# Kernel optimization log

Hardware: AMD Instinct MI355X
Metric: run time of the kernel (lower is better)

## Reference

```python
import jax, jax.numpy as jnp
import numpy as np

B, T, S, D, H, F, L = 4, 512, 512, 1024, 16, 4096, 2
VOCAB, MAXC = 32000, 1024
PAD, CONCEPT, DBPEDIA, USER = 0, 1, 2, 3
EPS = 1e-5
NEG = -1e20


def _ln(x):
    # LayerNorm (gamma=1, beta=0 at init, as in nn.LayerNorm defaults)
    m = jnp.mean(x, axis=-1, keepdims=True)
    v = jnp.mean((x - m) ** 2, axis=-1, keepdims=True)
    return (x - m) / jnp.sqrt(v + EPS)


def _mha(q_in, kv, mask, Wq, bq, Wk, bk, Wv, bv, Wo, bo):
    # q_in: [B,T,D]; kv: [B,K,D]; mask: broadcastable to [B,H,T,K] (bool)
    dh = D // H

    def heads(x, W, b):
        y = x @ W + b
        return y.reshape(x.shape[0], x.shape[1], H, dh).transpose(0, 2, 1, 3)

    q = heads(q_in, Wq, bq) / jnp.sqrt(jnp.asarray(dh, q_in.dtype))
    k = heads(kv, Wk, bk)
    v = heads(kv, Wv, bv)
    scores = jnp.einsum('bhqd,bhkd->bhqk', q, k)
    # original: dot_prod *= mask; masked_fill(mask==0, -NEAR_INF) == where(mask, s, NEG)
    scores = jnp.where(mask, scores, NEG)
    w = jax.nn.softmax(scores, axis=-1)
    out = jnp.einsum('bhqk,bhkd->bhqd', w, v)
    out = out.transpose(0, 2, 1, 3).reshape(q_in.shape[0], q_in.shape[1], D)
    return out @ Wo + bo


def setup_inputs() -> dict:
    key = jax.random.key(0)
    ks = jax.random.split(key, 16)
    w = 0.02
    return {
        'sum_embeddings': jax.random.normal(ks[0], (VOCAB, D), jnp.float32),
        'predict_vector': jax.random.randint(ks[1], (B, T), 0, VOCAB),
        'encoder_latent_emb': jax.random.normal(ks[2], (B, S, D), jnp.float32),
        'con_graph_fc_emb': jax.random.normal(ks[3], (B, S, D), jnp.float32),
        'db_graph_fc_emb': jax.random.normal(ks[4], (B, S, D), jnp.float32),
        'user_graph_fc_emb': jax.random.normal(ks[5], (B, S, D), jnp.float32),
        'context_mask': jax.random.randint(ks[6], (B, S), 0, 5),
        'pos_emb': jax.random.normal(ks[7], (MAXC, D), jnp.float32) * (D ** -0.5),
        'attn_Wq': jax.random.normal(ks[8], (L, 5, D, D), jnp.float32) * w,
        'attn_bq': jnp.zeros((L, 5, D), jnp.float32),
        'attn_Wk': jax.random.normal(ks[9], (L, 5, D, D), jnp.float32) * w,
        'attn_bk': jnp.zeros((L, 5, D), jnp.float32),
        'attn_Wv': jax.random.normal(ks[10], (L, 5, D, D), jnp.float32) * w,
        'attn_bv': jnp.zeros((L, 5, D), jnp.float32),
        'attn_Wo': jax.random.normal(ks[11], (L, 5, D, D), jnp.float32) * w,
        'attn_bo': jnp.zeros((L, 5, D), jnp.float32),
        'ffn_W1': jax.random.normal(ks[12], (L, D, F), jnp.float32) * w,
        'ffn_b1': jnp.zeros((L, F), jnp.float32),
        'ffn_W2': jax.random.normal(ks[13], (L, F, D), jnp.float32) * w,
        'ffn_b2': jnp.zeros((L, D), jnp.float32),
    }


def reference(sum_embeddings, predict_vector, encoder_latent_emb, con_graph_fc_emb,
              db_graph_fc_emb, user_graph_fc_emb, context_mask, pos_emb,
              attn_Wq, attn_bq, attn_Wk, attn_bk, attn_Wv, attn_bv, attn_Wo, attn_bo,
              ffn_W1, ffn_b1, ffn_W2, ffn_b2):
    enc_mask = (context_mask != PAD)[:, None, None, :]      # [B,1,1,S]
    con_mask = (context_mask != CONCEPT)[:, None, None, :]
    db_mask = (context_mask != DBPEDIA)[:, None, None, :]
    user_mask = (context_mask != USER)[:, None, None, :]
    dec_mask = jnp.tril(jnp.ones((T, T), bool))[None, None]  # causal [1,1,T,T]

    x = sum_embeddings[predict_vector] * jnp.sqrt(jnp.asarray(D, jnp.float32))
    x = x + pos_emb[:T][None]
    x = _ln(x)  # dropout is identity at inference

    for l in range(L):
        def att(i, q, kv, m):
            return _mha(q, kv, m,
                        attn_Wq[l, i], attn_bq[l, i], attn_Wk[l, i], attn_bk[l, i],
                        attn_Wv[l, i], attn_bv[l, i], attn_Wo[l, i], attn_bo[l, i])
        x = _ln(x + att(0, x, x, dec_mask))                      # self
        x = _ln(x + att(1, x, db_graph_fc_emb, db_mask))         # db
        x = _ln(x + att(2, x, con_graph_fc_emb, con_mask))       # kg/concept
        x = _ln(x + att(3, x, user_graph_fc_emb, user_mask))     # user
        x = _ln(x + att(4, x, encoder_latent_emb, enc_mask))     # encoder
        h = jax.nn.relu(x @ ffn_W1[l] + ffn_b1[l]) @ ffn_W2[l] + ffn_b2[l]
        x = _ln(x + h)
    return x
```

## Files before the change

kernel.cpp:

```cpp
#include <hip/hip_runtime.h>

#define BB  4
#define TT  512
#define DD  1024
#define HH  16
#define DHH 64
#define FF  4096

typedef unsigned short u16;
typedef __attribute__((ext_vector_type(8))) short bfrag8;
typedef __attribute__((ext_vector_type(4))) float facc4;

__device__ __forceinline__ u16 f2bf(float f){
  unsigned u = __float_as_uint(f);
  unsigned r = u + 0x7fffu + ((u >> 16) & 1u);
  return (u16)(r >> 16);
}
__device__ __forceinline__ float bf2f(u16 h){
  return __uint_as_float(((unsigned)h) << 16);
}

__device__ __forceinline__ void gload16(const u16* g, u16* l){
  __builtin_amdgcn_global_load_lds(
      (const __attribute__((address_space(1))) void*)g,
      (__attribute__((address_space(3))) void*)l, 16, 0, 0);
}

template<int N> __device__ __forceinline__ void vwait(){
  static_assert(N==0 || N==4 || N==6 || N==8 || N==12, "bad vmcnt literal");
  if constexpr (N==0)  asm volatile("s_waitcnt vmcnt(0)" ::: "memory");
  else if constexpr (N==4)  asm volatile("s_waitcnt vmcnt(4)" ::: "memory");
  else if constexpr (N==6)  asm volatile("s_waitcnt vmcnt(6)" ::: "memory");
  else if constexpr (N==8)  asm volatile("s_waitcnt vmcnt(8)" ::: "memory");
  else if constexpr (N==12) asm volatile("s_waitcnt vmcnt(12)" ::: "memory");
}

__global__ __launch_bounds__(256) void prep_all(
    const float* __restrict__ Wq, const float* __restrict__ Wk,
    const float* __restrict__ Wv, const float* __restrict__ Wo,
    const float* __restrict__ W1, const float* __restrict__ W2,
    const float* __restrict__ g_db, const float* __restrict__ g_con,
    const float* __restrict__ g_usr, const float* __restrict__ g_enc,
    u16* __restrict__ dst0,
    u16* __restrict__ kvb0, u16* __restrict__ kvb1,
    u16* __restrict__ kvb2, u16* __restrict__ kvb3,
    const float* __restrict__ emb, const int* __restrict__ pvec,
    const float* __restrict__ pos, u16* __restrict__ xbout)
{
  const int fid = blockIdx.x;
  const int bid = (fid < 14336) ? ((fid & 7) * 1792 + (fid >> 3)) : fid;
  const int tid = threadIdx.x;
  if (bid >= 22528){
    const int row = bid - 22528;
    const int lane = tid & 63, wid = tid >> 6;
    const int idx = pvec[row];
    const int t = row & (TT - 1);
    float4 e = ((const float4*)(emb + (long)idx * DD))[tid];
    float4 p = ((const float4*)(pos + (long)t * DD))[tid];
    float4 x;
    x.x = e.x * 32.0f + p.x; x.y = e.y * 32.0f + p.y;
    x.z = e.z * 32.0f + p.z; x.w = e.w * 32.0f + p.w;
    float s = x.x + x.y + x.z + x.w;
    #pragma unroll
    for (int o = 32; o; o >>= 1) s += __shfl_xor(s, o);
    __shared__ float red[4];
    if (lane == 0) red[wid] = s;
    __syncthreads();
    const float mean = (red[0] + red[1] + red[2] + red[3]) * (1.0f / DD);
    __syncthreads();
    const float dx = x.x - mean, dy = x.y - mean, dz = x.z - mean, dw = x.w - mean;
    float q = dx*dx + dy*dy + dz*dz + dw*dw;
    #pragma unroll
    for (int o = 32; o; o >>= 1) q += __shfl_xor(q, o);
    if (lane == 0) red[wid] = q;
    __syncthreads();
    const float var = (red[0] + red[1] + red[2] + red[3]) * (1.0f / DD);
    const float rstd = rsqrtf(var + 1e-5f);
    ushort4 o4;
    o4.x = f2bf(dx*rstd); o4.y = f2bf(dy*rstd);
    o4.z = f2bf(dz*rstd); o4.w = f2bf(dw*rstd);
    ((ushort4*)(xbout + (long)row * DD))[tid] = o4;
    return;
  }
  if (bid >= 14336){
    const int r = bid - 14336;
    const float* s; u16* d;
    switch (r >> 11){
      case 0: s = g_db;  d = kvb0; break;
      case 1: s = g_con; d = kvb1; break;
      case 2: s = g_usr; d = kvb2; break;
      default: s = g_enc; d = kvb3; break;
    }
    const int i = (r & 2047) * 256 + tid;
    float4 v = ((const float4*)s)[i];
    ushort4 o;
    o.x = f2bf(v.x); o.y = f2bf(v.y); o.z = f2bf(v.z); o.w = f2bf(v.w);
    ((ushort4*)d)[i] = o;
    return;
  }
  constexpr long D2 = (long)DD * DD, DF = (long)DD * FF;
  constexpr long O_Wproj = 0, O_WkvC = 14*D2, O_WoT = 30*D2,
                 O_W1T = 40*D2, O_W2T = 40*D2 + 2*DF;
  const float* src; long soff, doff; int R, C, rem;
  if (bid < 1536){
    const int j = bid / 512;
    src = (j==0) ? Wq : (j==1) ? Wk : Wv;
    const int l = (bid % 512) / 256; rem = bid & 255;
    soff = (long)l * 5 * D2;
    doff = O_Wproj + (long)l * 7 * D2 +
           ((j==0) ? 0L : (j==1) ? 5L*D2 : 6L*D2);
    R = DD; C = DD;
  } else if (bid < 5632){
    const int idx = (bid - 1536) >> 8; rem = bid & 255;
    const int l = idx >> 3, ci = (idx >> 1) & 3, kv = idx & 1;
    src = kv ? Wv : Wk;
    soff = (long)(l*5 + 1 + ci) * D2;
    doff = O_WkvC + (long)(l*8 + ci*2 + kv) * D2;
    R = DD; C = DD;
  } else if (bid < 7680){
    const int idx = (bid - 5632) >> 8; rem = bid & 255;
    const int l = idx >> 2, ci = idx & 3;
    src = Wq;
    soff = (long)(l*5 + 1 + ci) * D2;
    doff = O_Wproj + (long)l * 7 * D2 + (long)(1 + ci) * D2;
    R = DD; C = DD;
  } else if (bid < 10240){
    const int idx = (bid - 7680) >> 8; rem = bid & 255;
    src = Wo; soff = (long)idx * D2; doff = O_WoT + (long)idx * D2;
    R = DD; C = DD;
  } else if (bid < 12288){
    const int b5 = bid - 10240;
    const int z = b5 >> 10; rem = b5 & 1023;
    src = W1; soff = (long)z * DF; doff = O_W1T + (long)z * DF;
    R = DD; C = FF;
  } else {
    const int b6 = bid - 12288;
    const int z = b6 >> 10; rem = b6 & 1023;
    src = W2; soff = (long)z * DF; doff = O_W2T + (long)z * DF;
    R = FF; C = DD;
  }
  const int ctiles = C >> 6;
  const int c0 = (rem % ctiles) << 6;
  const int r0 = (rem / ctiles) << 6;

  __shared__ u16 tile[64][66];
  const int tr = tid >> 4, tc = tid & 15;
  #pragma unroll
  for (int i = 0; i < 4; ++i){
    const int row = tr + i*16;
    float4 v = ((const float4*)(src + soff + (long)(r0 + row)*C + c0))[tc];
    unsigned* t32 = (unsigned*)&tile[row][tc*4];
    t32[0] = (unsigned)f2bf(v.x) | ((unsigned)f2bf(v.y) << 16);
    t32[1] = (unsigned)f2bf(v.z) | ((unsigned)f2bf(v.w) << 16);
  }
  __syncthreads();
  const int ch = tid & 7;
  const int cb = tid >> 3;
  #pragma unroll
  for (int it = 0; it < 2; ++it){
    const int cc = cb + it*32;
    union { int4 v; u16 u[8]; } P;
    #pragma unroll
    for (int j = 0; j < 8; ++j) P.u[j] = tile[ch*8 + j][cc];
    *(int4*)&dst0[doff + (long)(c0 + cc)*R + r0 + ch*8] = P.v;
  }
}

__global__ __launch_bounds__(256) void ln_chain5(
    const float* __restrict__ o5, u16* __restrict__ xb)
{
  const int row = blockIdx.x;
  const int i = threadIdx.x;
  const int lane = i & 63, wid = i >> 6;
  __shared__ float red[4];
  constexpr long NB = (long)2048 * 1024;
  ushort4 x4 = ((const ushort4*)(xb + (long)row * DD))[i];
  float4 x;
  x.x = bf2f(x4.x); x.y = bf2f(x4.y); x.z = bf2f(x4.z); x.w = bf2f(x4.w);
  #pragma unroll
  for (int it = 0; it < 5; ++it){
    float4 o = ((const float4*)(o5 + (long)it * NB + (long)row * DD))[i];
    x.x += o.x; x.y += o.y; x.z += o.z; x.w += o.w;
    float s = x.x + x.y + x.z + x.w;
    #pragma unroll
    for (int off = 32; off; off >>= 1) s += __shfl_xor(s, off);
    if (lane == 0) red[wid] = s;
    __syncthreads();
    const float mean = (red[0] + red[1] + red[2] + red[3]) * (1.0f / DD);
    __syncthreads();
    x.x -= mean; x.y -= mean; x.z -= mean; x.w -= mean;
    float q = x.x*x.x + x.y*x.y + x.z*x.z + x.w*x.w;
    #pragma unroll
    for (int off = 32; off; off >>= 1) q += __shfl_xor(q, off);
    if (lane == 0) red[wid] = q;
    __syncthreads();
    const float var = (red[0] + red[1] + red[2] + red[3]) * (1.0f / DD);
    const float rstd = rsqrtf(var + 1e-5f);
    x.x *= rstd; x.y *= rstd; x.z *= rstd; x.w *= rstd;
    __syncthreads();
  }
  ushort4 o4;
  o4.x = f2bf(x.x); o4.y = f2bf(x.y); o4.z = f2bf(x.z); o4.w = f2bf(x.w);
  ((ushort4*)(xb + (long)row * DD))[i] = o4;
}

__global__ __launch_bounds__(256) void ln_kernel(
    const float* __restrict__ a,
    float* __restrict__ yf, u16* __restrict__ yb)
{
  const int row = blockIdx.x;
  const int i = threadIdx.x;
  const int lane = i & 63, wid = i >> 6;
  float4 x = ((const float4*)(a + (long)row * DD))[i];
  float s = x.x + x.y + x.z + x.w;
  #pragma unroll
  for (int o = 32; o; o >>= 1) s += __shfl_xor(s, o);
  __shared__ float red[4];
  if (lane == 0) red[wid] = s;
  __syncthreads();
  const float mean = (red[0] + red[1] + red[2] + red[3]) * (1.0f / DD);
  __syncthreads();
  const float dx = x.x - mean, dy = x.y - mean, dz = x.z - mean, dw = x.w - mean;
  float q = dx*dx + dy*dy + dz*dz + dw*dw;
  #pragma unroll
  for (int o = 32; o; o >>= 1) q += __shfl_xor(q, o);
  if (lane == 0) red[wid] = q;
  __syncthreads();
  const float var = (red[0] + red[1] + red[2] + red[3]) * (1.0f / DD);
  const float rstd = rsqrtf(var + 1e-5f);
  float4 y; y.x = dx*rstd; y.y = dy*rstd; y.z = dz*rstd; y.w = dw*rstd;
  if (yf) ((float4*)(yf + (long)row * DD))[i] = y;
  if (yb){
    ushort4 o4; o4.x = f2bf(y.x); o4.y = f2bf(y.y); o4.z = f2bf(y.z); o4.w = f2bf(y.w);
    ((ushort4*)(yb + (long)row * DD))[i] = o4;
  }
}

template<bool CAUSAL>
__device__ __forceinline__ void flash_body(
    const u16* Q, const u16* Kt, const u16* Vt,
    const float* biasS, u16* O,
    int qt, int bh, u16 (*Ks)[64*64], u16 (*Vs)[64*64], u16* Ps)
{
  const int b = bh >> 4, h = bh & 15;
  const int tid = threadIdx.x, lane = tid & 63, wid = tid >> 6;
  const int fr = lane & 15, kg = lane >> 4;
  const int srow = tid >> 3;
  const int gcol = ((tid & 7) ^ (srow & 7)) * 8;
  u16* Pw = Ps + wid * 1024;
  const facc4 z4 = {0.0f, 0.0f, 0.0f, 0.0f};

  const long base = (long)bh * (512 * 64);
  const u16* qrow = Q + base + (long)(qt*64 + wid*16 + fr) * 64;
  const bfrag8 aq0 = *(const bfrag8*)(qrow + kg*8);
  const bfrag8 aq1 = *(const bfrag8*)(qrow + 32 + kg*8);

  auto stageKV = [&](int buf, int kt){
    u16* Kd = Ks[buf] + wid * 512;
    u16* Vd = Vs[buf] + wid * 512;
    #pragma unroll
    for (int p = 0; p < 2; ++p)
      gload16(Kt + base + (long)(kt*64 + p*32 + srow) * 64 + gcol, Kd + p*2048);
    #pragma unroll
    for (int p = 0; p < 2; ++p)
      gload16(Vt + base + (long)(p*32 + srow) * 512 + kt*64 + gcol, Vd + p*2048);
  };

  float mrow[4], lrow[4];
  #pragma unroll
  for (int r = 0; r < 4; ++r){ mrow[r] = -3e38f; lrow[r] = 0.0f; }
  facc4 accO[4] = {};

  const int NT = CAUSAL ? (qt + 1) : 8;
  stageKV(0, 0);
  if (NT > 1){ stageKV(1, 1); vwait<4>(); }
  else vwait<0>();
  __builtin_amdgcn_s_barrier();

  for (int kt = 0; kt < NT; ++kt){
    const int cur = kt & 1;
    bfrag8 bk[4][2], bv[4][2];
    #pragma unroll
    for (int j = 0; j < 4; ++j)
      #pragma unroll
      for (int c2 = 0; c2 < 2; ++c2){
        const int po = (((c2*4 + kg) ^ (fr & 7)) * 8);
        bk[j][c2] = *(const bfrag8*)&Ks[cur][(j*16 + fr)*64 + po];
        bv[j][c2] = *(const bfrag8*)&Vs[cur][(j*16 + fr)*64 + po];
      }
    __builtin_amdgcn_sched_barrier(0);
    __builtin_amdgcn_s_barrier();
    if (kt + 2 < NT){ stageKV(cur, kt + 2); vwait<4>(); }
    else vwait<0>();
    __builtin_amdgcn_s_barrier();

    facc4 sc[4];
    __builtin_amdgcn_s_setprio(1);
    #pragma unroll
    for (int j = 0; j < 4; ++j){
      sc[j] = __builtin_amdgcn_mfma_f32_16x16x32_bf16(aq0, bk[j][0], z4, 0, 0, 0);
      sc[j] = __builtin_amdgcn_mfma_f32_16x16x32_bf16(aq1, bk[j][1], sc[j], 0, 0, 0);
    }
    __builtin_amdgcn_s_setprio(0);
    if (CAUSAL){
      const int rowb = qt*64 + wid*16 + kg*4;
      #pragma unroll
      for (int j = 0; j < 4; ++j){
        const int col = kt*64 + j*16 + fr;
        #pragma unroll
        for (int r = 0; r < 4; ++r)
          if (col > rowb + r) sc[j][r] = -1e20f;
      }
    } else {
      #pragma unroll
      for (int j = 0; j < 4; ++j){
        const float bval = biasS[kt*64 + j*16 + fr];
        #pragma unroll
        for (int r = 0; r < 4; ++r) sc[j][r] += bval;
      }
    }
    float tmax[4];
    #pragma unroll
    for (int r = 0; r < 4; ++r)
      tmax[r] = fmaxf(fmaxf(sc[0][r], sc[1][r]), fmaxf(sc[2][r], sc[3][r]));
    #pragma unroll
    for (int o = 1; o < 16; o <<= 1)
      #pragma unroll
      for (int r = 0; r < 4; ++r)
        tmax[r] = fmaxf(tmax[r], __shfl_xor(tmax[r], o));
    bool grow = false;
    #pragma unroll
    for (int r = 0; r < 4; ++r) grow = grow || (tmax[r] > mrow[r] + 8.0f);
    if (__any(grow)){
      float fac[4];
      #pragma unroll
      for (int r = 0; r < 4; ++r){
        const float mn = fmaxf(mrow[r], tmax[r]);
        fac[r] = __expf(mrow[r] - mn);
        mrow[r] = mn;
        lrow[r] *= fac[r];
      }
      #pragma unroll
      for (int f = 0; f < 4; ++f)
        #pragma unroll
        for (int r = 0; r < 4; ++r) accO[f][r] *= fac[r];
    }
    float tsum[4] = {0.0f, 0.0f, 0.0f, 0.0f};
    #pragma unroll
    for (int j = 0; j < 4; ++j)
      #pragma unroll
      for (int r = 0; r < 4; ++r){
        const float p = __expf(sc[j][r] - mrow[r]);
        sc[j][r] = p; tsum[r] += p;
      }
    #pragma unroll
    for (int o = 1; o < 16; o <<= 1)
      #pragma unroll
      for (int r = 0; r < 4; ++r) tsum[r] += __shfl_xor(tsum[r], o);
    #pragma unroll
    for (int r = 0; r < 4; ++r) lrow[r] += tsum[r];

    #pragma unroll
    for (int j = 0; j < 4; ++j)
      #pragma unroll
      for (int r = 0; r < 4; ++r){
        const int row = kg*4 + r;
        const int col = j*16 + fr;
        Pw[row*64 + (((col >> 3) ^ (row & 7)) * 8) + (col & 7)] = f2bf(sc[j][r]);
      }
    bfrag8 ap[2];
    #pragma unroll
    for (int c2 = 0; c2 < 2; ++c2)
      ap[c2] = *(const bfrag8*)&Pw[fr*64 + (((c2*4 + kg) ^ (fr & 7)) * 8)];
    __builtin_amdgcn_s_setprio(1);
    #pragma unroll
    for (int f = 0; f < 4; ++f){
      accO[f] = __builtin_amdgcn_mfma_f32_16x16x32_bf16(ap[0], bv[f][0], accO[f], 0, 0, 0);
      accO[f] = __builtin_amdgcn_mfma_f32_16x16x32_bf16(ap[1], bv[f][1], accO[f], 0, 0, 0);
    }
    __builtin_amdgcn_s_setprio(0);
  }

  #pragma unroll
  for (int f = 0; f < 4; ++f)
    #pragma unroll
    for (int r = 0; r < 4; ++r){
      const int row = kg*4 + r;
      const int col = f*16 + fr;
      Pw[(row*64 + col) ^ ((row & 7) << 3)] = f2bf(accO[f][r] / lrow[r]);
    }
  const int prow = lane >> 2, pch = lane & 3;
  const long orow = (long)(b*512 + qt*64 + wid*16 + prow) * 1024 + h*64;
  #pragma unroll
  for (int it2 = 0; it2 < 2; ++it2){
    const int ch2 = pch + it2*4;
    int4 w4 = *(const int4*)&Pw[(prow*64 + ch2*8) ^ ((prow & 7) << 3)];
    *(int4*)&O[orow + ch2*8] = w4;
  }
}

__global__ __launch_bounds__(256, 3) void flash_all5(
    const u16* __restrict__ Qb5, const u16* __restrict__ Kb,
    const u16* __restrict__ Vtb, const u16* __restrict__ KVcl,
    const int* __restrict__ cmask, u16* __restrict__ O5)
{
  __shared__ __align__(16) u16 Ks[2][64*64];
  __shared__ __align__(16) u16 Vs[2][64*64];
  __shared__ __align__(16) u16 Ps[4*16*64];
  __shared__ float biasS[512];
  const int z = blockIdx.z;
  const int fid = blockIdx.y * 8 + blockIdx.x;
  const int lid = (fid & 7) * 64 + (fid >> 3);
  const int qt = lid & 7, bh = lid >> 3;
  constexpr long NB = (long)2048 * 1024;
  if (z == 0){
    flash_body<true>(Qb5, Kb, Vtb, nullptr, O5, qt, bh, Ks, Vs, Ps);
  } else {
    const int ci = z - 1;
    const int mode = (0x0312 >> (ci*4)) & 0xF;
    const int b = bh >> 4;
    const int tid = threadIdx.x;
    #pragma unroll
    for (int r = 0; r < 2; ++r){
      const int c = r * 256 + tid;
      biasS[c] = (cmask[b * 512 + c] != mode) ? 0.0f : -1e20f;
    }
    __syncthreads();
    flash_body<false>(Qb5 + (long)z * NB,
                      KVcl + (long)(ci*2) * NB, KVcl + (long)(ci*2 + 1) * NB,
                      biasS, O5 + (long)z * NB, qt, bh, Ks, Vs, Ps);
  }
}

#define MODE_F32   0
#define MODE_BF16  1
#define MODE_KV    4
#define MODE_PROJ  6
#define MODE_F32B  7

__device__ __forceinline__ long qk_off(int gm, int gn){
  return (((long)(gm >> 9) * HH + (gn >> 6)) * TT + (gm & (TT-1))) * DHH + (gn & (DHH-1));
}

template<int BM, int BN, int MODE>
__global__ __launch_bounds__(256, 2) void gemm_k(
    const u16* __restrict__ A, const u16* __restrict__ B,
    const float* __restrict__ bias0, const float* __restrict__ bias1,
    const float* __restrict__ bias2,
    float* __restrict__ Cf, u16* __restrict__ Cb0, u16* __restrict__ Cb1,
    u16* __restrict__ Cb2, const u16* __restrict__ resb,
    int K, int lda, int ldb, int ldc,
    int relu, float alpha)
{
  constexpr int BK = 64;
  constexpr int NBUF = (BM == 64 && BN == 64) ? 3 : 2;
  constexpr int ASZ = BM * BK, BSZ = BN * BK;
  __shared__ __align__(16) u16 As[NBUF * ASZ];
  __shared__ __align__(16) u16 Bs[NBUF * BSZ];

  const int gx = gridDim.x, gy = gridDim.y;
  const int nwg = gx * gy * gridDim.z;
  const int fid = (blockIdx.z * gy + blockIdx.y) * gx + blockIdx.x;
  const int cpx = nwg >> 3;
  const int lid = (fid & 7) * cpx + (fid >> 3);
  const int bx = lid % gx;
  const int rem = lid / gx;
  const int by = rem % gy;
  const int z  = rem / gy;

  const u16* Ab;
  const u16* Bb;
  long cbase;
  constexpr long NBA = (long)2048 * 1024;
  constexpr long D2C = (long)DD * DD;
  if constexpr (MODE == MODE_KV){
    const int ci = z >> 2, ll = (z >> 1) & 1, isv = z & 1;
    Ab = A + (long)ci * NBA;
    Bb = B + (long)(ll*8 + ci*2 + isv) * D2C;
    cbase = (long)(ll*8 + ci*2 + isv) * NBA;
  } else if constexpr (MODE == MODE_F32B){
    Ab = A + (long)z * NBA;
    Bb = B + (long)z * D2C;
    cbase = (long)z * NBA;
  } else {
    Ab = A; Bb = B; cbase = 0;
  }
  const int tid = threadIdx.x, lane = tid & 63, wid = tid >> 6;
  const int m0 = by * BM, n0 = bx * BN;
  constexpr int TMW = BM / 2, TNW = BN / 2;
  constexpr int FM = TMW / 16, FN = TNW / 16;
  const int wm = (wid >> 1) * TMW, wn = (wid & 1) * TNW;
  const int fr = lane & 15, kg = lane >> 4;
  facc4 acc[FM][FN] = {};

  const int srow = tid >> 3;
  const int gcol = (((tid & 7) ^ (srow & 7)) * 8);
  constexpr int AP = BM / 32, BP = BN / 32;
  constexpr int LPS = AP + BP;

  auto stage = [&](int buf, int k0){
    u16* Ad = As + buf * ASZ + wid * 512;
    u16* Bd = Bs + buf * BSZ + wid * 512;
    #pragma unroll
    for (int p = 0; p < AP; ++p)
      gload16(Ab + (long)(m0 + p*32 + srow) * lda + (k0 + gcol), Ad + p*2048);
    #pragma unroll
    for (int p = 0; p < BP; ++p)
      gload16(Bb + (long)(n0 + p*32 + srow) * ldb + (k0 + gcol), Bd + p*2048);
  };

  const int nsteps = K / BK;
  stage(0, 0);
  if constexpr (NBUF == 3){
    if (nsteps > 1) stage(1, BK);
    if (nsteps > 2) stage(2, 2*BK);
    if (nsteps > 2) vwait<2*LPS>();
    else if (nsteps > 1) vwait<LPS>();
    else vwait<0>();
  } else {
    if (nsteps > 1){ stage(1, BK); vwait<LPS>(); }
    else vwait<0>();
  }
  __builtin_amdgcn_s_barrier();

  int cur = 0;
  for (int s = 0; s < nsteps; ++s){
    const u16* Ar = As + cur * ASZ;
    const u16* Br = Bs + cur * BSZ;
    bfrag8 af[FM][2], bfv[FN][2];
    #pragma unroll
    for (int i = 0; i < FM; ++i)
      #pragma unroll
      for (int c2 = 0; c2 < 2; ++c2)
        af[i][c2] = *(const bfrag8*)&Ar[(wm + i*16 + fr) * 64 + (((c2*4 + kg) ^ (fr & 7)) * 8)];
    #pragma unroll
    for (int j = 0; j < FN; ++j)
      #pragma unroll
      for (int c2 = 0; c2 < 2; ++c2)
        bfv[j][c2] = *(const bfrag8*)&Br[(wn + j*16 + fr) * 64 + (((c2*4 + kg) ^ (fr & 7)) * 8)];
    __builtin_amdgcn_sched_barrier(0);
    __builtin_amdgcn_s_barrier();
    if constexpr (NBUF == 3){
      if (s + 3 < nsteps){ stage(cur, (s + 3) * BK); vwait<2*LPS>(); }
      else if (s + 2 < nsteps) vwait<LPS>();
      else if (s + 1 < nsteps) vwait<0>();
    } else {
      if (s + 2 < nsteps){ stage(cur, (s + 2) * BK); vwait<LPS>(); }
      else if (s + 1 < nsteps) vwait<0>();
    }
    __builtin_amdgcn_s_barrier();
    #pragma unroll
    for (int i = 0; i < FM; ++i)
      #pragma unroll
      for (int j = 0; j < FN; ++j){
        acc[i][j] = __builtin_amdgcn_mfma_f32_16x16x32_bf16(af[i][0], bfv[j][0], acc[i][j], 0, 0, 0);
        acc[i][j] = __builtin_amdgcn_mfma_f32_16x16x32_bf16(af[i][1], bfv[j][1], acc[i][j], 0, 0, 0);
      }
    cur = (cur == NBUF - 1) ? 0 : cur + 1;
  }

  if constexpr (MODE == MODE_KV || MODE == MODE_PROJ){
    const float* vb = nullptr; u16* vdst = nullptr; int n0e = 0; bool vpath = false;
    if constexpr (MODE == MODE_KV){
      const int ci = z >> 2, ll = (z >> 1) & 1, isv = z & 1;
      if (isv){ vpath = true; vb = bias1 + (long)(ll*5 + ci + 1) * DD; vdst = Cb0 + cbase; n0e = n0; }
    } else {
      if ((n0 >> 10) == 6){ vpath = true; vb = bias2; vdst = Cb2; n0e = n0 - 6144; }
    }
    if (vpath){
      u16* S = Bs;
      #pragma unroll
      for (int j = 0; j < FN; ++j){
        const int nl = wn + j*16 + fr;
        const float bvv = vb[n0e + nl];
        #pragma unroll
        for (int i = 0; i < FM; ++i)
          #pragma unroll
          for (int rr = 0; rr < 4; ++rr){
            const int ml = wm + i*16 + kg*4 + rr;
            S[(nl*BM + ml) ^ ((nl & 7) << 3)] = f2bf(acc[i][j][rr] + bvv);
          }
      }
      __syncthreads();
      constexpr int TPR = 256 / BN;
      constexpr int CPT = BM / (8 * TPR);
      const int n = tid / TPR;
      const int mh = (tid % TPR) * (BM / TPR);
      const long rowoff = (((long)(m0 >> 9) * HH + ((n0e + n) >> 6)) * DHH
                           + ((n0e + n) & 63)) * TT + (m0 & 511) + mh;
      #pragma unroll
      for (int c = 0; c < CPT; ++c){
        int4 w4 = *(const int4*)&S[(n*BM + mh + c*8) ^ ((n & 7) << 3)];
        *(int4*)&vdst[rowoff + c*8] = w4;
      }
      return;
    }
  }

  if constexpr (MODE == MODE_BF16 || MODE == MODE_PROJ || MODE == MODE_KV){
    u16* S = As;
    const float* bp = bias0;
    float sc2 = alpha;
    u16* dst = Cb0;
    int nb = 0;
    constexpr long NBA2 = (long)2048 * 1024;
    if constexpr (MODE == MODE_KV){
      const int ci = z >> 2, ll = (z >> 1) & 1;
      bp = bias0 + (long)(ll*5 + ci + 1) * DD;
    } else if constexpr (MODE == MODE_PROJ){
      const int sect = n0 >> 10;
      nb = n0 & 1023;
      if (sect <= 4){ bp = bias0 + (long)sect * DD; sc2 = 0.125f; dst = Cb0 + (long)sect * NBA2; }
      else          { bp = bias1; sc2 = 1.0f; dst = Cb1; }
    }
    #pragma unroll
    for (int i = 0; i < FM; ++i)
      #pragma unroll
      for (int j = 0; j < FN; ++j){
        const int nl = wn + j*16 + fr;
        float bvv;
        if constexpr (MODE == MODE_PROJ) bvv = bp[nb + nl];
        else bvv = bp ? bp[n0 + nl] : 0.0f;
        #pragma unroll
        for (int rr = 0; rr < 4; ++rr){
          const int ml = wm + i*16 + kg*4 + rr;
          float v = (acc[i][j][rr] + bvv) * sc2;
          if (relu) v = fmaxf(v, 0.0f);
          S[(ml*BN + nl) ^ ((ml & 7) << 3)] = f2bf(v);
        }
      }
    __syncthreads();
    constexpr int CPR = BN / 8;
    constexpr int NIT = (BM * CPR) / 256;
    #pragma unroll
    for (int it = 0; it < NIT; ++it){
      const int idx = it * 256 + tid;
      const int row = idx / CPR, ch = idx % CPR;
      int4 w4 = *(const int4*)&S[(row*BN + ch*8) ^ ((row & 7) << 3)];
      const int gm = m0 + row;
      long off;
      if constexpr (MODE == MODE_BF16) off = cbase + (long)gm * ldc + (n0 + ch*8);
      else if constexpr (MODE == MODE_PROJ) off = qk_off(gm, nb + ch*8);
      else off = cbase + qk_off(gm, n0 + ch*8);
      *(int4*)&dst[off] = w4;
    }
    return;
  }

  {
    const float* bp0 = bias0;
    if constexpr (MODE == MODE_F32B) bp0 = bias0 + (long)z * DD;
    #pragma unroll
    for (int i = 0; i < FM; ++i){
      #pragma unroll
      for (int j = 0; j < FN; ++j){
        const int gn = n0 + wn + j*16 + fr;
        #pragma unroll
        for (int rr = 0; rr < 4; ++rr){
          const int gm = m0 + wm + i*16 + kg*4 + rr;
          float v = acc[i][j][rr];
          v = (v + (bp0 ? bp0[gn] : 0.0f)) * alpha;
          if (relu) v = fmaxf(v, 0.0f);
          const long off = cbase + (long)gm * ldc + gn;
          if constexpr (MODE == MODE_F32){
            if (resb) v += bf2f(resb[off]);
          }
          Cf[off] = v;
        }
      }
    }
  }
}

extern "C" void kernel_launch(void* const* d_in, const int* in_sizes, int n_in,
                              void* d_out, int out_size, void* d_ws, size_t ws_size,
                              hipStream_t stream)
{
  (void)in_sizes; (void)n_in; (void)out_size; (void)ws_size;
  const float* emb   = (const float*)d_in[0];
  const int*   pvec  = (const int*)d_in[1];
  const float* g_enc = (const float*)d_in[2];
  const float* g_con = (const float*)d_in[3];
  const float* g_db  = (const float*)d_in[4];
  const float* g_usr = (const float*)d_in[5];
  const int*   cmask = (const int*)d_in[6];
  const float* pose  = (const float*)d_in[7];
  const float* Wq = (const float*)d_in[8];
  const float* bq = (const float*)d_in[9];
  const float* Wk = (const float*)d_in[10];
  const float* bk = (const float*)d_in[11];
  const float* Wv = (const float*)d_in[12];
  const float* bv = (const float*)d_in[13];
  const float* Wo = (const float*)d_in[14];
  const float* bo = (const float*)d_in[15];
  const float* W1 = (const float*)d_in[16];
  const float* b1 = (const float*)d_in[17];
  const float* W2 = (const float*)d_in[18];
  const float* b2 = (const float*)d_in[19];
  float* out = (float*)d_out;

  const size_t NTOK = (size_t)BB * TT;
  const long D2 = (long)DD * DD;

  char* wp = (char*)d_ws;
  auto alloc = [&](size_t bytes) -> char* {
    char* p = wp;
    wp += (bytes + 255) & ~(size_t)255;
    return p;
  };
  u16*   WprojT = (u16*) alloc(sizeof(u16) * 2 * 7 * D2);
  u16*   WkvC   = (u16*) alloc(sizeof(u16) * 2 * 4 * 2 * D2);
  u16*   WoT    = (u16*) alloc(sizeof(u16) * 10 * D2);
  u16*   W1T    = (u16*) alloc(sizeof(u16) * 2 * DD * FF);
  u16*   W2T    = (u16*) alloc(sizeof(u16) * 2 * DD * FF);
  u16*   kvb0  = (u16*)  alloc(sizeof(u16) * NTOK * DD);
  u16*   kvb1  = (u16*)  alloc(sizeof(u16) * NTOK * DD);
  u16*   kvb2  = (u16*)  alloc(sizeof(u16) * NTOK * DD);
  u16*   kvb3  = (u16*)  alloc(sizeof(u16) * NTOK * DD);
  u16*   KVc   = (u16*)  alloc(sizeof(u16) * 16 * NTOK * DD);
  u16*   xb    = (u16*)  alloc(sizeof(u16) * NTOK * DD);
  u16*   Qb5   = (u16*)  alloc(sizeof(u16) * 5 * NTOK * DD);
  u16*   Kb    = (u16*)  alloc(sizeof(u16) * NTOK * DD);
  u16*   Vtb   = (u16*)  alloc(sizeof(u16) * NTOK * DD);
  u16*   attnb5= (u16*)  alloc(sizeof(u16) * 5 * NTOK * DD);
  float* oproj5= (float*)alloc(sizeof(float) * 5 * NTOK * DD);
  float* obuf  = (float*)alloc(sizeof(float) * NTOK * DD);
  u16*   hb    = (u16*)  alloc(sizeof(u16) * NTOK * FF);

  prep_all<<<24576, 256, 0, stream>>>(
      Wq, Wk, Wv, Wo, W1, W2, g_db, g_con, g_usr, g_enc,
      (u16*)d_ws, kvb0, kvb1, kvb2, kvb3,
      emb, pvec, pose, xb);

  const long NB = (long)NTOK * DD;
  gemm_k<128,128,MODE_KV><<<dim3(8,16,16), 256, 0, stream>>>(
    kvb0, WkvC, bk, bv, nullptr,
    nullptr, KVc, nullptr, nullptr, nullptr,
    DD, DD, DD, 0, 0, 1.0f);

  for (int l = 0; l < 2; ++l){
    gemm_k<128,128,MODE_PROJ><<<dim3(56,16,1), 256, 0, stream>>>(
      xb, WprojT + (long)l*7*D2,
      bq + (size_t)l*5*DD, bk + (size_t)l*5*DD, bv + (size_t)l*5*DD,
      nullptr, Qb5, Kb, Vtb, nullptr,
      DD, DD, DD, 0, 0, 1.0f);

    flash_all5<<<dim3(8,64,5), 256, 0, stream>>>(
        Qb5, Kb, Vtb, KVc + (long)l*8*NB, cmask, attnb5);

    gemm_k<128,128,MODE_F32B><<<dim3(8,16,5), 256, 0, stream>>>(
      attnb5, WoT + (long)l*5*D2,
      bo + (size_t)l*5*DD, nullptr, nullptr,
      oproj5, nullptr, nullptr, nullptr, nullptr,
      DD, DD, DD, DD, 0, 1.0f);

    ln_chain5<<<(int)NTOK, 256, 0, stream>>>(oproj5, xb);

    gemm_k<128,128,MODE_BF16><<<dim3(32,16,1), 256, 0, stream>>>(
      xb, W1T + (size_t)l*DD*FF,
      b1 + (size_t)l*FF, nullptr, nullptr,
      nullptr, hb, nullptr, nullptr, nullptr,
      DD, DD, DD, FF, 1, 1.0f);
    gemm_k<64,64,MODE_F32><<<dim3(16,32,1), 256, 0, stream>>>(
      hb, W2T + (size_t)l*DD*FF,
      b2 + (size_t)l*DD, nullptr, nullptr,
      obuf, nullptr, nullptr, nullptr, xb,
      FF, FF, FF, DD, 0, 1.0f);
    float* yf = (l == 1) ? out : nullptr;
    ln_kernel<<<(int)NTOK, 256, 0, stream>>>(obuf, yf, (l == 1) ? nullptr : xb);
  }
}
```

Measured before the change: 675.4 us.

## Replace KV projection GEMM with 256x256-tile 8-wave pipelined kernel

Moves the batched K/V projection GEMM for the cross-attention memories out of the generic 128x128 gemm_k template into a dedicated kernel. The new kernel uses 256x256 tiles, 512 threads (8 waves), double-buffered LDS and a hand-interleaved schedule of LDS reads, MFMA quarters and global-to-LDS prefetches, with explicit barriers and raised wave priority around MFMA bursts. The larger tiles cut global/LDS traffic per FLOP but reduce grid size to 512 blocks and use 128KB of LDS, which limits occupancy and puts the whole schedule on hand-tuned barriers.

```diff
diff --git a/kernel.cpp b/kernel.cpp
--- a/kernel.cpp
+++ b/kernel.cpp
@@ -434,12 +434,201 @@
 
 #define MODE_F32   0
 #define MODE_BF16  1
-#define MODE_KV    4
 #define MODE_PROJ  6
 #define MODE_F32B  7
 
 __device__ __forceinline__ long qk_off(int gm, int gn){
   return (((long)(gm >> 9) * HH + (gn >> 6)) * TT + (gm & (TT-1))) * DHH + (gn & (DHH-1));
+}
+
+__global__ __launch_bounds__(512, 2) void gemm256_kv(
+    const u16* __restrict__ A, const u16* __restrict__ B,
+    const float* __restrict__ bkb, const float* __restrict__ bvb,
+    u16* __restrict__ Cb)
+{
+  __shared__ __align__(16) u16 lds[65536];
+
+  const int gx = gridDim.x, gy = gridDim.y;
+  const int nwg = gx * gy * gridDim.z;
+  const int fid = (blockIdx.z * gy + blockIdx.y) * gx + blockIdx.x;
+  const int cpx = nwg >> 3;
+  const int lid = (fid & 7) * cpx + (fid >> 3);
+  const int bx = lid % gx;
+  const int rem = lid / gx;
+  const int by = rem % gy;
+  const int z  = rem / gy;
+
+  constexpr long NBA = (long)2048 * 1024;
+  constexpr long D2C = (long)DD * DD;
+  const int ci = z >> 2, ll = (z >> 1) & 1, isv = z & 1;
+  const u16* Ab = A + (long)ci * NBA;
+  const u16* Bb = B + (long)(ll*8 + ci*2 + isv) * D2C;
+  const long cbase = (long)(ll*8 + ci*2 + isv) * NBA;
+
+  const int tid = threadIdx.x, lane = tid & 63, w = tid >> 6;
+  const int m0 = by * 256, n0 = bx * 256;
+  const int wmh = w >> 2;
+  const int wn  = w & 3;
+  const int bhf = wn >> 1;
+  const int brow0 = (wn & 1) * 64;
+  const int fr = lane & 15, kg = lane >> 4;
+  facc4 acc[8][4] = {};
+
+  const int sr8 = (tid >> 3) & 7;
+  const int sgc = ((tid & 7) ^ sr8) * 8;
+
+  auto stageA = [&](int buf, int h, int t){
+    u16* d = lds + (buf*2 + h) * 8192 + tid * 8;
+    #pragma unroll
+    for (int p = 0; p < 2; ++p)
+      gload16(Ab + (long)(m0 + h*128 + p*64 + (tid >> 3)) * DD + t*64 + sgc,
+              d + p*4096);
+  };
+  auto stageB = [&](int buf, int h, int t){
+    u16* d = lds + 32768 + (buf*2 + h) * 8192 + tid * 8;
+    #pragma unroll
+    for (int p = 0; p < 2; ++p)
+      gload16(Bb + (long)(n0 + h*128 + p*64 + (tid >> 3)) * DD + t*64 + sgc,
+              d + p*4096);
+  };
+
+  bfrag8 af[4][2], bf[4][2];
+  auto readA = [&](int buf, int mg){
+    const u16* Ah = lds + (buf*2 + wmh) * 8192;
+    #pragma unroll
+    for (int q = 0; q < 4; ++q){
+      const int row = (mg*4 + q)*16 + fr;
+      #pragma unroll
+      for (int c2 = 0; c2 < 2; ++c2)
+        af[q][c2] = *(const bfrag8*)&Ah[row*64 + (((c2*4 + kg) ^ (fr & 7)) * 8)];
+    }
+  };
+  auto readB = [&](int buf, int ng){
+    const u16* Bh = lds + 32768 + (buf*2 + bhf) * 8192;
+    #pragma unroll
+    for (int q = 0; q < 2; ++q){
+      const int row = brow0 + (ng*2 + q)*16 + fr;
+      #pragma unroll
+      for (int c2 = 0; c2 < 2; ++c2)
+        bf[ng*2 + q][c2] = *(const bfrag8*)&Bh[row*64 + (((c2*4 + kg) ^ (fr & 7)) * 8)];
+    }
+  };
+  auto mmaQ = [&](int mg, int ng){
+    __builtin_amdgcn_s_setprio(1);
+    #pragma unroll
+    for (int q = 0; q < 4; ++q)
+      #pragma unroll
+      for (int r2 = 0; r2 < 2; ++r2){
+        const int i = mg*4 + q, j = ng*2 + r2;
+        acc[i][j] = __builtin_amdgcn_mfma_f32_16x16x32_bf16(af[q][0], bf[j][0], acc[i][j], 0, 0, 0);
+        acc[i][j] = __builtin_amdgcn_mfma_f32_16x16x32_bf16(af[q][1], bf[j][1], acc[i][j], 0, 0, 0);
+      }
+    __builtin_amdgcn_s_setprio(0);
+  };
+
+  stageB(0,0,0); stageB(0,1,0); stageA(0,0,0); stageA(0,1,0);
+  stageB(1,0,1); stageB(1,1,1); stageA(1,0,1); stageA(1,1,1);
+  vwait<8>();
+  __builtin_amdgcn_s_barrier();
+
+  for (int J = 0; J < 8; ++J){
+    const int t2 = 2*J + 2, t3 = 2*J + 3;
+    const bool pf = (J < 7);
+    readA(0, 0); readB(0, 0);
+    __builtin_amdgcn_sched_barrier(0);
+    __builtin_amdgcn_s_barrier();
+    mmaQ(0, 0);
+    __builtin_amdgcn_s_barrier();
+    readB(0, 1);
+    __builtin_amdgcn_sched_barrier(0);
+    __builtin_amdgcn_s_barrier();
+    mmaQ(0, 1);
+    __builtin_amdgcn_s_barrier();
+    readA(0, 1);
+    if (pf) stageB(0, 0, t2);
+    __builtin_amdgcn_sched_barrier(0);
+    __builtin_amdgcn_s_barrier();
+    mmaQ(1, 0);
+    __builtin_amdgcn_s_barrier();
+    if (pf){ stageB(0, 1, t2); vwait<4>(); }
+    else vwait<0>();
+    __builtin_amdgcn_s_barrier();
+    mmaQ(1, 1);
+    __builtin_amdgcn_s_barrier();
+    readA(1, 0); readB(1, 0);
+    if (pf){ stageA(0, 0, t2); stageA(0, 1, t2); }
+    __builtin_amdgcn_sched_barrier(0);
+    __builtin_amdgcn_s_barrier();
+    mmaQ(0, 0);
+    __builtin_amdgcn_s_barrier();
+    readB(1, 1);
+    __builtin_amdgcn_sched_barrier(0);
+    __builtin_amdgcn_s_barrier();
+    mmaQ(0, 1);
+    __builtin_amdgcn_s_barrier();
+    readA(1, 1);
+    if (pf) stageB(1, 0, t3);
+    __builtin_amdgcn_sched_barrier(0);
+    __builtin_amdgcn_s_barrier();
+    mmaQ(1, 0);
+    __builtin_amdgcn_s_barrier();
+    if (pf){ stageB(1, 1, t3); stageA(1, 0, t3); stageA(1, 1, t3); }
+    vwait<6>();
+    __builtin_amdgcn_s_barrier();
+    mmaQ(1, 1);
+    __builtin_amdgcn_s_barrier();
+  }
+  __syncthreads();
+
+  u16* S = lds;
+  if (isv){
+    const float* vb = bvb + (long)(ll*5 + ci + 1) * DD;
+    #pragma unroll
+    for (int j = 0; j < 4; ++j){
+      const int nl = wn*64 + j*16 + fr;
+      const float bvv = vb[n0 + nl];
+      #pragma unroll
+      for (int i = 0; i < 8; ++i)
+        #pragma unroll
+        for (int rr = 0; rr < 4; ++rr){
+          const int ml = wmh*128 + i*16 + kg*4 + rr;
+          S[(nl*256 + ml) ^ ((nl & 7) << 3)] = f2bf(acc[i][j][rr] + bvv);
+        }
+    }
+    __syncthreads();
+    const int n = tid >> 1;
+    const int mh = (tid & 1) * 128;
+    const long rowoff = (((long)(m0 >> 9) * HH + ((n0 + n) >> 6)) * DHH
+                         + ((n0 + n) & 63)) * TT + (m0 & 511) + mh;
+    u16* vdst = Cb + cbase;
+    #pragma unroll
+    for (int c = 0; c < 16; ++c){
+      int4 w4 = *(const int4*)&S[(n*256 + mh + c*8) ^ ((n & 7) << 3)];
+      *(int4*)&vdst[rowoff + c*8] = w4;
+    }
+  } else {
+    const float* bp = bkb + (long)(ll*5 + ci + 1) * DD;
+    #pragma unroll
+    for (int i = 0; i < 8; ++i)
+      #pragma unroll
+      for (int j = 0; j < 4; ++j){
+        const int nl = wn*64 + j*16 + fr;
+        const float bvv = bp[n0 + nl];
+        #pragma unroll
+        for (int rr = 0; rr < 4; ++rr){
+          const int ml = wmh*128 + i*16 + kg*4 + rr;
+          S[(ml*256 + nl) ^ ((ml & 7) << 3)] = f2bf(acc[i][j][rr] + bvv);
+        }
+      }
+    __syncthreads();
+    #pragma unroll
+    for (int it = 0; it < 16; ++it){
+      const int idx = it * 512 + tid;
+      const int row = idx >> 5, ch = idx & 31;
+      int4 w4 = *(const int4*)&S[(row*256 + ch*8) ^ ((row & 7) << 3)];
+      *(int4*)&Cb[cbase + qk_off(m0 + row, n0 + ch*8)] = w4;
+    }
+  }
 }
 
 template<int BM, int BN, int MODE>
@@ -473,12 +662,7 @@
   long cbase;
   constexpr long NBA = (long)2048 * 1024;
   constexpr long D2C = (long)DD * DD;
-  if constexpr (MODE == MODE_KV){
-    const int ci = z >> 2, ll = (z >> 1) & 1, isv = z & 1;
-    Ab = A + (long)ci * NBA;
-    Bb = B + (long)(ll*8 + ci*2 + isv) * D2C;
-    cbase = (long)(ll*8 + ci*2 + isv) * NBA;
-  } else if constexpr (MODE == MODE_F32B){
+  if constexpr (MODE == MODE_F32B){
     Ab = A + (long)z * NBA;
     Bb = B + (long)z * D2C;
     cbase = (long)z * NBA;
@@ -559,15 +743,11 @@
     cur = (cur == NBUF - 1) ? 0 : cur + 1;
   }
 
-  if constexpr (MODE == MODE_KV || MODE == MODE_PROJ){
-    const float* vb = nullptr; u16* vdst = nullptr; int n0e = 0; bool vpath = false;
-    if constexpr (MODE == MODE_KV){
-      const int ci = z >> 2, ll = (z >> 1) & 1, isv = z & 1;
-      if (isv){ vpath = true; vb = bias1 + (long)(ll*5 + ci + 1) * DD; vdst = Cb0 + cbase; n0e = n0; }
-    } else {
-      if ((n0 >> 10) == 6){ vpath = true; vb = bias2; vdst = Cb2; n0e = n0 - 6144; }
-    }
-    if (vpath){
+  if constexpr (MODE == MODE_PROJ){
+    if ((n0 >> 10) == 6){
+      const float* vb = bias2;
+      u16* vdst = Cb2;
+      const int n0e = n0 - 6144;
       u16* S = Bs;
       #pragma unroll
       for (int j = 0; j < FN; ++j){
@@ -597,17 +777,14 @@
     }
   }
 
-  if constexpr (MODE == MODE_BF16 || MODE == MODE_PROJ || MODE == MODE_KV){
+  if constexpr (MODE == MODE_BF16 || MODE == MODE_PROJ){
     u16* S = As;
     const float* bp = bias0;
     float sc2 = alpha;
     u16* dst = Cb0;
     int nb = 0;
     constexpr long NBA2 = (long)2048 * 1024;
-    if constexpr (MODE == MODE_KV){
-      const int ci = z >> 2, ll = (z >> 1) & 1;
-      bp = bias0 + (long)(ll*5 + ci + 1) * DD;
-    } else if constexpr (MODE == MODE_PROJ){
+    if constexpr (MODE == MODE_PROJ){
       const int sect = n0 >> 10;
       nb = n0 & 1023;
       if (sect <= 4){ bp = bias0 + (long)sect * DD; sc2 = 0.125f; dst = Cb0 + (long)sect * NBA2; }
@@ -640,8 +817,7 @@
       const int gm = m0 + row;
       long off;
       if constexpr (MODE == MODE_BF16) off = cbase + (long)gm * ldc + (n0 + ch*8);
-      else if constexpr (MODE == MODE_PROJ) off = qk_off(gm, nb + ch*8);
-      else off = cbase + qk_off(gm, n0 + ch*8);
+      else off = qk_off(gm, nb + ch*8);
       *(int4*)&dst[off] = w4;
     }
     return;
@@ -733,10 +909,7 @@
       emb, pvec, pose, xb);
 
   const long NB = (long)NTOK * DD;
-  gemm_k<128,128,MODE_KV><<<dim3(8,16,16), 256, 0, stream>>>(
-    kvb0, WkvC, bk, bv, nullptr,
-    nullptr, KVc, nullptr, nullptr, nullptr,
-    DD, DD, DD, 0, 0, 1.0f);
+  gemm256_kv<<<dim3(4,8,16), 512, 0, stream>>>(kvb0, WkvC, bk, bv, KVc);
 
   for (int l = 0; l < 2; ++l){
     gemm_k<128,128,MODE_PROJ><<<dim3(56,16,1), 256, 0, stream>>>(
```

Result: no change. 672.5 us (-0.4%).
